# Optimization experiments

Hardware: AMD Instinct MI355X
Metric: run time of the kernel (lower is better)

## Reference

```python
import jax, jax.numpy as jnp
import numpy as np

E, H, KVH, D = 2048, 16, 4, 128      # embed_dim, heads, kv heads, head_dim
HG, R, SYM, VAN = 12, 32, 4, 4       # graph heads, rel_rank, sym heads, vanilla heads
BASE = 10000
EPS = 1e-6


def _rms_norm(x, w):
    # RMSNorm over last dim (head_dim)
    return x * jax.lax.rsqrt(jnp.mean(x * x, axis=-1, keepdims=True) + EPS) * w


def _rotate_half(x):
    x1, x2 = jnp.split(x, 2, axis=-1)
    return jnp.concatenate([-x2, x1], axis=-1)


def _rope(q, k):
    # q, k: [B, H, S, D]
    S = q.shape[2]
    inv_freq = 1.0 / (BASE ** (jnp.arange(0, D, 2, dtype=jnp.float32) / D))
    t = jnp.arange(S, dtype=jnp.float32)
    freqs = jnp.outer(t, inv_freq)                       # [S, D/2]
    emb = jnp.concatenate([freqs, freqs], axis=-1)       # [S, D]
    cos = jnp.cos(emb)[None, None].astype(q.dtype)
    sin = jnp.sin(emb)[None, None].astype(q.dtype)
    return q * cos + _rotate_half(q) * sin, k * cos + _rotate_half(k) * sin


def setup_inputs() -> dict:
    key = jax.random.key(0)
    ks = jax.random.split(key, 9)
    B, S = 1, 2048
    std = 0.02
    return {
        'x': jax.random.normal(ks[0], (B, S, E), jnp.float32),
        'Wq': jax.random.normal(ks[1], (E, E), jnp.float32) * std,
        'Wk': jax.random.normal(ks[2], (KVH * D, E), jnp.float32) * std,
        'Wv': jax.random.normal(ks[3], (KVH * D, E), jnp.float32) * std,
        'Wo': jax.random.normal(ks[4], (E, E), jnp.float32) * std,
        'q_norm_w': jnp.ones((D,), jnp.float32),
        'k_norm_w': jnp.ones((D,), jnp.float32),
        'Wrq': jax.random.normal(ks[5], (HG * R, E), jnp.float32) * 0.01,
        'Wrk': jax.random.normal(ks[6], (HG * R, E), jnp.float32) * 0.01,
        'graph_scale': jax.random.normal(ks[7], (HG,), jnp.float32) * 0.1,
    }


def reference(x, Wq, Wk, Wv, Wo, q_norm_w, k_norm_w, Wrq, Wrk, graph_scale):
    B, S, _ = x.shape
    # projections -> [B, heads, S, D]
    q = (x @ Wq.T).reshape(B, S, H, D).transpose(0, 2, 1, 3)
    k = (x @ Wk.T).reshape(B, S, KVH, D).transpose(0, 2, 1, 3)
    v = (x @ Wv.T).reshape(B, S, KVH, D).transpose(0, 2, 1, 3)
    # QK-norm then RoPE
    q = _rms_norm(q, q_norm_w)
    k = _rms_norm(k, k_norm_w)
    q, k = _rope(q, k)
    # GQA: repeat kv heads
    rep = H // KVH
    k = jnp.repeat(k, rep, axis=1)
    v = jnp.repeat(v, rep, axis=1)
    # low-rank graph bias: [B, HG, S, S]
    Rq = (x @ Wrq.T).reshape(B, S, HG, R).transpose(0, 2, 1, 3)
    Rk = (x @ Wrk.T).reshape(B, S, HG, R).transpose(0, 2, 1, 3)
    bias = jnp.einsum('bhsr,bhtr->bhst', Rq, Rk)
    sym = bias[:, :SYM]
    sym = (sym + sym.transpose(0, 1, 3, 2)) * 0.5
    bias = jnp.concatenate([sym, bias[:, SYM:]], axis=1)
    bias = bias * graph_scale[None, :, None, None]
    # vanilla heads (last VAN heads) get zero bias
    bias = jnp.concatenate([bias, jnp.zeros((B, VAN, S, S), bias.dtype)], axis=1)
    # attention with causal mask
    scale = 1.0 / np.sqrt(D).astype(np.float32)
    scores = jnp.einsum('bhsd,bhtd->bhst', q, k) * scale + bias
    causal = jnp.tril(jnp.ones((S, S), bool))
    scores = jnp.where(causal[None, None], scores, jnp.finfo(scores.dtype).min)
    attn = jax.nn.softmax(scores, axis=-1)
    out = jnp.einsum('bhst,bhtd->bhsd', attn, v)
    out = out.transpose(0, 2, 1, 3).reshape(B, S, E)
    return out @ Wo.T
```

## Files before the change

kernel.cpp:

```cpp
#include <hip/hip_runtime.h>
#include <hip/hip_bf16.h>

typedef __attribute__((ext_vector_type(8))) short short8;
typedef __attribute__((ext_vector_type(4))) float f32x4;
typedef __attribute__((ext_vector_type(4))) unsigned int u32x4;

__device__ __forceinline__ f32x4 mfma16(short8 a, short8 b, f32x4 c) {
  return __builtin_amdgcn_mfma_f32_16x16x32_bf16(a, b, c, 0, 0, 0);
}

__device__ __forceinline__ void gload_lds16(const void* g, void* l) {
  __builtin_amdgcn_global_load_lds(
      (const __attribute__((address_space(1))) void*)g,
      (__attribute__((address_space(3))) void*)l, 16, 0, 0);
}

__device__ __forceinline__ unsigned int bfp(float lo, float hi) {
  return (unsigned int)__builtin_bit_cast(unsigned short, __float2bfloat16(lo)) |
         ((unsigned int)__builtin_bit_cast(unsigned short, __float2bfloat16(hi)) << 16);
}

struct __align__(8) bh4 { __hip_bfloat16 a, b, c, d; };
struct CastSeg { const float* src; __hip_bfloat16* dst; int n4; };
struct CastArgs { CastSeg seg[7]; int tot4; };

__global__ __launch_bounds__(256) void cast_all(CastArgs a) {
  int i = blockIdx.x * 256 + threadIdx.x;
  const int stride = gridDim.x * 256;
  for (; i < a.tot4; i += stride) {
    int j = i, s = 0;
    while (j >= a.seg[s].n4) { j -= a.seg[s].n4; ++s; }
    float4 v = ((const float4*)a.seg[s].src)[j];
    bh4 o{__float2bfloat16(v.x), __float2bfloat16(v.y),
          __float2bfloat16(v.z), __float2bfloat16(v.w)};
    ((bh4*)a.seg[s].dst)[j] = o;
  }
}

__global__ __launch_bounds__(256) void gemm_bt(const __hip_bfloat16* __restrict__ A,
                                               const __hip_bfloat16* __restrict__ B,
                                               float* __restrict__ C,
                                               int N, int K) {
  __shared__ __align__(16) __hip_bfloat16 As[64][32];
  __shared__ __align__(16) __hip_bfloat16 Bs[128][32];

  const int tid = threadIdx.x;
  const int lane = tid & 63, wv = tid >> 6;
  const int wn = wv * 32;
  const int l15 = lane & 15, g = lane >> 4;
  const int mb = blockIdx.y * 64, nb = blockIdx.x * 128;

  const int arow = wv * 16 + (lane >> 2);
  const int brow = wv * 32 + (lane >> 2);
  const int scol = (lane & 3) * 8;
  const __hip_bfloat16* Ap = A + (size_t)(mb + arow) * K + scol;
  const __hip_bfloat16* Bp = B + (size_t)(nb + brow) * K + scol;
  __hip_bfloat16* lA  = &As[wv * 16][0];
  __hip_bfloat16* lB0 = &Bs[wv * 32][0];
  __hip_bfloat16* lB1 = &Bs[wv * 32 + 16][0];

  const f32x4 zf = {0.f, 0.f, 0.f, 0.f};
  f32x4 acc[4][2];
#pragma unroll
  for (int m = 0; m < 4; ++m)
#pragma unroll
    for (int n = 0; n < 2; ++n) acc[m][n] = zf;

  for (int k0 = 0; k0 < K; k0 += 32) {
    __syncthreads();
    gload_lds16(Ap + k0, lA);
    gload_lds16(Bp + k0, lB0);
    gload_lds16(Bp + (size_t)16 * K + k0, lB1);
    __syncthreads();
    short8 af[4], bf[2];
#pragma unroll
    for (int m = 0; m < 4; ++m) af[m] = *(const short8*)&As[m * 16 + l15][g * 8];
#pragma unroll
    for (int n = 0; n < 2; ++n) bf[n] = *(const short8*)&Bs[wn + n * 16 + l15][g * 8];
#pragma unroll
    for (int m = 0; m < 4; ++m)
#pragma unroll
      for (int n = 0; n < 2; ++n) acc[m][n] = mfma16(af[m], bf[n], acc[m][n]);
  }

#pragma unroll
  for (int m = 0; m < 4; ++m)
#pragma unroll
    for (int n = 0; n < 2; ++n)
#pragma unroll
      for (int r = 0; r < 4; ++r)
        C[(size_t)(mb + m * 16 + g * 4 + r) * N + (nb + wn + n * 16 + l15)] =
            acc[m][n][r];
}

__global__ __launch_bounds__(256) void postproc(const float* __restrict__ C1,
                                                const float* __restrict__ qw,
                                                const float* __restrict__ kw,
                                                __hip_bfloat16* __restrict__ qn,
                                                __hip_bfloat16* __restrict__ kn,
                                                __hip_bfloat16* __restrict__ vt,
                                                __hip_bfloat16* __restrict__ rq,
                                                __hip_bfloat16* __restrict__ rk) {
  constexpr int S = 2048;
  const int s = blockIdx.x;
  const int tid = threadIdx.x;
  const int lane = tid & 63;
  const int wv = tid >> 6;
  const float* row = C1 + (size_t)s * 3840;

  const float f = exp2f(-(float)lane * (13.287712379549449f / 64.0f));
  const float ang = (float)s * f;
  float sn, cs;
  sincosf(ang, &sn, &cs);

  for (int hr = wv; hr < 20; hr += 4) {
    const float* base;
    __hip_bfloat16* dst;
    const float* nw;
    float oscale;
    if (hr < 16) {
      base = row + hr * 128;
      dst = qn + ((size_t)hr * S + s) * 128;
      nw = qw;
      oscale = 0.08838834764831845f;
    } else {
      const int h4 = hr - 16;
      base = row + 2048 + h4 * 128;
      dst = kn + ((size_t)h4 * S + s) * 128;
      nw = kw;
      oscale = 1.0f;
    }
    const float x1 = base[lane], x2 = base[lane + 64];
    float ss = x1 * x1 + x2 * x2;
#pragma unroll
    for (int mk = 1; mk < 64; mk <<= 1) ss += __shfl_xor(ss, mk);
    const float rms = rsqrtf(ss * (1.0f / 128.0f) + 1e-6f);
    const float x1n = x1 * rms * nw[lane];
    const float x2n = x2 * rms * nw[lane + 64];
    dst[lane]      = __float2bfloat16((x1n * cs - x2n * sn) * oscale);
    dst[lane + 64] = __float2bfloat16((x2n * cs + x1n * sn) * oscale);
  }
  for (int i = tid; i < 512; i += 256) {
    const int h4 = i >> 7, d = i & 127;
    vt[((size_t)h4 * 128 + d) * S + s] = __float2bfloat16(row[2560 + i]);
  }
  for (int i = tid; i < 768; i += 256) {
    if (i < 384) {
      rq[((size_t)(i >> 5) * S + s) * 32 + (i & 31)] = __float2bfloat16(row[3072 + i]);
    } else {
      const int j = i - 384;
      rk[((size_t)(j >> 5) * S + s) * 32 + (j & 31)] = __float2bfloat16(row[3072 + i]);
    }
  }
}

__global__ __launch_bounds__(256) void attn_kernel(
    const __hip_bfloat16* __restrict__ qn, const __hip_bfloat16* __restrict__ kn,
    const __hip_bfloat16* __restrict__ vt, const __hip_bfloat16* __restrict__ rq,
    const __hip_bfloat16* __restrict__ rk, const float* __restrict__ gsc,
    __hip_bfloat16* __restrict__ ao) {
  constexpr int S = 2048;
  constexpr float L2E = 1.4426950408889634f;
  const int bid = blockIdx.x;
  const int j = bid & 15;
  const int h = ((j & 3) << 2) | (j >> 2);
  const int u = bid >> 4;
  const int qb = (u < 16) ? (31 - u) : (u - 16);
  const int lane = threadIdx.x & 63;
  const int wv = threadIdx.x >> 6;
  const int qs = qb * 64 + wv * 16;
  const int l15 = lane & 15, g = lane >> 4;
  const int h4 = h >> 2;
  const bool has_bias = (h < 12);
  const bool symh = (h < 4);
  const float gs = has_bias ? gsc[h] : 0.0f;
  const f32x4 zf = {0.f, 0.f, 0.f, 0.f};

  short8 qf[4];
  {
    const __hip_bfloat16* qrow = qn + ((size_t)h * S + qs + l15) * 128 + g * 8;
#pragma unroll
    for (int kc = 0; kc < 4; ++kc) qf[kc] = *(const short8*)(qrow + kc * 32);
  }
  short8 rqA = {}, rkA = {};
  if (has_bias) rqA = *(const short8*)(rq + ((size_t)h * S + qs + l15) * 32 + g * 8);
  if (symh)     rkA = *(const short8*)(rk + ((size_t)h * S + qs + l15) * 32 + g * 8);

  const __hip_bfloat16* kbase = kn + (size_t)h4 * S * 128;
  const __hip_bfloat16* vbase = vt + (size_t)h4 * 128 * S;
  const __hip_bfloat16* rkp   = rk + (size_t)h * S * 32;
  const __hip_bfloat16* rqp   = rq + (size_t)h * S * 32;

  float lp = 0.0f;
  f32x4 acc[8];
#pragma unroll
  for (int fb = 0; fb < 8; ++fb) acc[fb] = zf;

  const int nt = qb + 1;

  short8 rkB[4], rqB[4];
  if (has_bias) {
#pragma unroll
    for (int tf = 0; tf < 4; ++tf)
      rkB[tf] = *(const short8*)(rkp + (size_t)(tf * 16 + l15) * 32 + g * 8);
    if (symh) {
#pragma unroll
      for (int tf = 0; tf < 4; ++tf)
        rqB[tf] = *(const short8*)(rqp + (size_t)(tf * 16 + l15) * 32 + g * 8);
    }
  }

  const int srcA = l15 + ((g & 1) << 5);
  const int srcB = srcA + 16;
  const bool ghi = (g >= 2);

  for (int t = 0; t < nt; ++t) {
    const int tbase = t * 64;

    f32x4 bias4[4];
    if (has_bias) {
#pragma unroll
      for (int tf = 0; tf < 4; ++tf) bias4[tf] = mfma16(rkB[tf], rqA, zf);
      if (symh) {
#pragma unroll
        for (int tf = 0; tf < 4; ++tf) {
          f32x4 b2 = mfma16(rqB[tf], rkA, zf);
#pragma unroll
          for (int r = 0; r < 4; ++r) bias4[tf][r] = 0.5f * (bias4[tf][r] + b2[r]);
        }
      }
      if (t + 1 < nt) {
        const int tb2 = tbase + 64;
#pragma unroll
        for (int tf = 0; tf < 4; ++tf)
          rkB[tf] = *(const short8*)(rkp + (size_t)(tb2 + tf * 16 + l15) * 32 + g * 8);
        if (symh) {
#pragma unroll
          for (int tf = 0; tf < 4; ++tf)
            rqB[tf] = *(const short8*)(rqp + (size_t)(tb2 + tf * 16 + l15) * 32 + g * 8);
        }
      }
    }

    f32x4 sc[4];
#pragma unroll
    for (int tf = 0; tf < 4; ++tf) {
      f32x4 s4 = zf;
      const __hip_bfloat16* krow = kbase + (size_t)(tbase + tf * 16 + l15) * 128 + g * 8;
#pragma unroll
      for (int kc = 0; kc < 4; ++kc) {
        short8 kf = *(const short8*)(krow + kc * 32);
        s4 = mfma16(kf, qf[kc], s4);
      }
#pragma unroll
      for (int r = 0; r < 4; ++r) {
        float sv = s4[r];
        if (has_bias) sv += gs * bias4[tf][r];
        if (tbase + tf * 16 + g * 4 + r > qs + l15) sv = -1e30f;
        const float p = exp2f(sv * L2E);
        lp += p;
        sc[tf][r] = p;
      }
    }

    unsigned int pk0[4], pk1[4];
#pragma unroll
    for (int tf = 0; tf < 4; ++tf) {
      pk0[tf] = bfp(sc[tf][0], sc[tf][1]);
      pk1[tf] = bfp(sc[tf][2], sc[tf][3]);
    }
    unsigned int a0[4], a1[4], b0[4], b1[4];
#pragma unroll
    for (int tf = 0; tf < 4; ++tf) {
      a0[tf] = __shfl(pk0[tf], srcA);
      a1[tf] = __shfl(pk1[tf], srcA);
      b0[tf] = __shfl(pk0[tf], srcB);
      b1[tf] = __shfl(pk1[tf], srcB);
    }
    u32x4 w0 = {ghi ? a0[1] : a0[0], ghi ? a1[1] : a1[0],
                ghi ? b0[1] : b0[0], ghi ? b1[1] : b1[0]};
    u32x4 w1 = {ghi ? a0[3] : a0[2], ghi ? a1[3] : a1[2],
                ghi ? b0[3] : b0[2], ghi ? b1[3] : b1[2]};
    const short8 pa0 = __builtin_bit_cast(short8, w0);
    const short8 pa1 = __builtin_bit_cast(short8, w1);

#pragma unroll
    for (int fb = 0; fb < 8; ++fb) {
      const __hip_bfloat16* vrow = vbase + (size_t)(fb * 16 + l15) * S + tbase + g * 8;
      short8 v0 = *(const short8*)(vrow);
      short8 v1 = *(const short8*)(vrow + 32);
      acc[fb] = mfma16(pa0, v0, acc[fb]);
      acc[fb] = mfma16(pa1, v1, acc[fb]);
    }
  }

  float lt = lp;
  lt += __shfl_xor(lt, 16);
  lt += __shfl_xor(lt, 32);
  const float linv = 1.0f / lt;
  float lr[4];
#pragma unroll
  for (int r = 0; r < 4; ++r) lr[r] = __shfl(linv, g * 4 + r);

#pragma unroll
  for (int fb = 0; fb < 8; ++fb)
#pragma unroll
    for (int r = 0; r < 4; ++r) {
      const int srow = qs + g * 4 + r;
      ao[(size_t)srow * 2048 + h * 128 + fb * 16 + l15] =
          __float2bfloat16(acc[fb][r] * lr[r]);
    }
}

extern "C" void kernel_launch(void* const* d_in, const int* in_sizes, int n_in,
                              void* d_out, int out_size, void* d_ws, size_t ws_size,
                              hipStream_t stream) {
  (void)in_sizes; (void)n_in; (void)out_size; (void)ws_size;
  constexpr int S = 2048, E = 2048;

  const float* x   = (const float*)d_in[0];
  const float* Wq  = (const float*)d_in[1];
  const float* Wk  = (const float*)d_in[2];
  const float* Wv  = (const float*)d_in[3];
  const float* Wo  = (const float*)d_in[4];
  const float* qw  = (const float*)d_in[5];
  const float* kw  = (const float*)d_in[6];
  const float* Wrq = (const float*)d_in[7];
  const float* Wrk = (const float*)d_in[8];
  const float* gsc = (const float*)d_in[9];
  float* out = (float*)d_out;

  char* ws = (char*)d_ws;
  size_t off = 0;
  auto alloc = [&](size_t bytes) -> void* {
    void* p = ws + off;
    off += (bytes + 255) & ~(size_t)255;
    return p;
  };
  __hip_bfloat16* xb   = (__hip_bfloat16*)alloc((size_t)S * E * 2);
  __hip_bfloat16* Wall = (__hip_bfloat16*)alloc((size_t)3840 * E * 2);
  __hip_bfloat16* Wob  = (__hip_bfloat16*)alloc((size_t)E * E * 2);
  __hip_bfloat16* qnb  = (__hip_bfloat16*)alloc((size_t)16 * S * 128 * 2);
  __hip_bfloat16* knb  = (__hip_bfloat16*)alloc((size_t)4 * S * 128 * 2);
  __hip_bfloat16* vtb  = (__hip_bfloat16*)alloc((size_t)4 * 128 * S * 2);
  __hip_bfloat16* rqb  = (__hip_bfloat16*)alloc((size_t)12 * S * 32 * 2);
  __hip_bfloat16* rkb  = (__hip_bfloat16*)alloc((size_t)12 * S * 32 * 2);
  float* C1            = (float*)alloc((size_t)S * 3840 * 4);
  __hip_bfloat16* ao   = (__hip_bfloat16*)C1;

  CastArgs ca;
  ca.seg[0] = {x,   xb,                      (int)((size_t)S * E / 4)};
  ca.seg[1] = {Wq,  Wall,                    (int)((size_t)E * E / 4)};
  ca.seg[2] = {Wk,  Wall + (size_t)2048 * E, (int)((size_t)512 * E / 4)};
  ca.seg[3] = {Wv,  Wall + (size_t)2560 * E, (int)((size_t)512 * E / 4)};
  ca.seg[4] = {Wrq, Wall + (size_t)3072 * E, (int)((size_t)384 * E / 4)};
  ca.seg[5] = {Wrk, Wall + (size_t)3456 * E, (int)((size_t)384 * E / 4)};
  ca.seg[6] = {Wo,  Wob,                     (int)((size_t)E * E / 4)};
  ca.tot4 = 0;
  for (int i = 0; i < 7; ++i) ca.tot4 += ca.seg[i].n4;
  cast_all<<<dim3(2048), dim3(256), 0, stream>>>(ca);

  gemm_bt<<<dim3(30, 32), dim3(256), 0, stream>>>(xb, Wall, C1, 3840, E);
  postproc<<<dim3(2048), dim3(256), 0, stream>>>(C1, qw, kw, qnb, knb, vtb, rqb, rkb);
  attn_kernel<<<dim3(512), dim3(256), 0, stream>>>(qnb, knb, vtb, rqb, rkb, gsc, ao);
  gemm_bt<<<dim3(16, 32), dim3(256), 0, stream>>>(ao, Wob, out, E, E);
}
```

Baseline: 359.2 us.

## Stage K/V tiles through double-buffered swizzled LDS with register prefetch

In the attention loop, each wave used to load K and V fragments straight from global memory, and the four waves of a block loaded the same tile redundantly. The block now loads each 64-key K/V tile cooperatively into registers one tile ahead, writes it into a double-buffered XOR-swizzled shared-memory buffer, and reads MFMA fragments from LDS. This cuts redundant global traffic and hides load latency behind compute. In exchange it adds 64KB of LDS per block, which can limit occupancy, plus a __syncthreads per iteration.

```diff
diff --git a/kernel.cpp b/kernel.cpp
--- a/kernel.cpp
+++ b/kernel.cpp
@@ -166,8 +166,9 @@
   const int h = ((j & 3) << 2) | (j >> 2);
   const int u = bid >> 4;
   const int qb = (u < 16) ? (31 - u) : (u - 16);
-  const int lane = threadIdx.x & 63;
-  const int wv = threadIdx.x >> 6;
+  const int tid = threadIdx.x;
+  const int lane = tid & 63;
+  const int wv = tid >> 6;
   const int qs = qb * 64 + wv * 16;
   const int l15 = lane & 15, g = lane >> 4;
   const int h4 = h >> 2;
@@ -176,27 +177,53 @@
   const float gs = has_bias ? gsc[h] : 0.0f;
   const f32x4 zf = {0.f, 0.f, 0.f, 0.f};
 
-  short8 qf[4];
-  {
-    const __hip_bfloat16* qrow = qn + ((size_t)h * S + qs + l15) * 128 + g * 8;
-#pragma unroll
-    for (int kc = 0; kc < 4; ++kc) qf[kc] = *(const short8*)(qrow + kc * 32);
-  }
-  short8 rqA = {}, rkA = {};
-  if (has_bias) rqA = *(const short8*)(rq + ((size_t)h * S + qs + l15) * 32 + g * 8);
-  if (symh)     rkA = *(const short8*)(rk + ((size_t)h * S + qs + l15) * 32 + g * 8);
+  __shared__ __align__(16) char KsRaw[2][16384];
+  __shared__ __align__(16) char VsRaw[2][16384];
+
+  const int sxk = ((tid >> 4) & 7) << 4;
+  const int sxv = ((tid >> 3) & 7) << 4;
+  const int k_wr = (tid * 16) ^ sxk;
+  const int v_wr = (tid * 16) ^ sxv;
+  const int kx = (l15 & 7) << 4;
 
   const __hip_bfloat16* kbase = kn + (size_t)h4 * S * 128;
   const __hip_bfloat16* vbase = vt + (size_t)h4 * 128 * S;
   const __hip_bfloat16* rkp   = rk + (size_t)h * S * 32;
   const __hip_bfloat16* rqp   = rq + (size_t)h * S * 32;
 
+  short8 qf[4];
+  {
+    const __hip_bfloat16* qrow = qn + ((size_t)h * S + qs + l15) * 128 + g * 8;
+#pragma unroll
+    for (int kc = 0; kc < 4; ++kc) qf[kc] = *(const short8*)(qrow + kc * 32);
+  }
+  short8 rqA = {}, rkA = {};
+  if (has_bias) rqA = *(const short8*)(rqp + (size_t)(qs + l15) * 32 + g * 8);
+  if (symh)     rkA = *(const short8*)(rkp + (size_t)(qs + l15) * 32 + g * 8);
+
   float lp = 0.0f;
   f32x4 acc[8];
 #pragma unroll
   for (int fb = 0; fb < 8; ++fb) acc[fb] = zf;
 
   const int nt = qb + 1;
+
+  short8 kreg[4], vreg[4];
+  auto load_kv = [&](int tb) {
+#pragma unroll
+    for (int c = 0; c < 4; ++c) {
+      kreg[c] = *(const short8*)(kbase + ((size_t)(tb + c * 16 + (tid >> 4))) * 128 + (tid & 15) * 8);
+      vreg[c] = *(const short8*)(vbase + ((size_t)(c * 32 + (tid >> 3))) * S + tb + (tid & 7) * 8);
+    }
+  };
+
+  load_kv(0);
+#pragma unroll
+  for (int c = 0; c < 4; ++c) {
+    *(short8*)(&KsRaw[0][c * 4096 + k_wr]) = kreg[c];
+    *(short8*)(&VsRaw[0][c * 4096 + v_wr]) = vreg[c];
+  }
+  if (nt > 1) load_kv(64);
 
   short8 rkB[4], rqB[4];
   if (has_bias) {
@@ -214,8 +241,24 @@
   const int srcB = srcA + 16;
   const bool ghi = (g >= 2);
 
+  __syncthreads();
+
   for (int t = 0; t < nt; ++t) {
     const int tbase = t * 64;
+    const int cur = t & 1;
+    const char* ksb = &KsRaw[cur][0];
+    const char* vsb = &VsRaw[cur][0];
+
+    if (t + 1 < nt) {
+      char* ksw = &KsRaw[cur ^ 1][0];
+      char* vsw = &VsRaw[cur ^ 1][0];
+#pragma unroll
+      for (int c = 0; c < 4; ++c) {
+        *(short8*)(ksw + c * 4096 + k_wr) = kreg[c];
+        *(short8*)(vsw + c * 4096 + v_wr) = vreg[c];
+      }
+      if (t + 2 < nt) load_kv(tbase + 128);
+    }
 
     f32x4 bias4[4];
     if (has_bias) {
@@ -246,10 +289,9 @@
 #pragma unroll
     for (int tf = 0; tf < 4; ++tf) {
       f32x4 s4 = zf;
-      const __hip_bfloat16* krow = kbase + (size_t)(tbase + tf * 16 + l15) * 128 + g * 8;
 #pragma unroll
       for (int kc = 0; kc < 4; ++kc) {
-        short8 kf = *(const short8*)(krow + kc * 32);
+        short8 kf = *(const short8*)(ksb + ((((tf * 16 + l15) << 8) + (kc << 6) + (g << 4)) ^ kx));
         s4 = mfma16(kf, qf[kc], s4);
       }
 #pragma unroll
@@ -286,12 +328,13 @@
 
 #pragma unroll
     for (int fb = 0; fb < 8; ++fb) {
-      const __hip_bfloat16* vrow = vbase + (size_t)(fb * 16 + l15) * S + tbase + g * 8;
-      short8 v0 = *(const short8*)(vrow);
-      short8 v1 = *(const short8*)(vrow + 32);
+      short8 v0 = *(const short8*)(vsb + ((((fb * 16 + l15) << 7) + (g << 4)) ^ kx));
+      short8 v1 = *(const short8*)(vsb + ((((fb * 16 + l15) << 7) + 64 + (g << 4)) ^ kx));
       acc[fb] = mfma16(pa0, v0, acc[fb]);
       acc[fb] = mfma16(pa1, v1, acc[fb]);
     }
+
+    __syncthreads();
   }
 
   float lt = lp;
```

New measurement: 312.4 us. 13.0% less time.
